# Performance work log

Measured on AMD Instinct MI355X. Metric: run time of the kernel, lower is better.

## Reference

```python
import jax, jax.numpy as jnp
import numpy as np

N_NODES = 50000
N_EDGES = 500000
IN_DIM = 128
H1, C1 = 4, 64   # layer1: heads=4, out=64, concat -> 256
H2, C2 = 1, 64   # layer2: heads=1, out=64


def setup_inputs() -> dict:
    key = jax.random.key(0)
    ks = jax.random.split(key, 16)
    p = lambda k, shp: (jax.random.normal(k, shp, dtype=jnp.float32) * 0.1)
    return {
        "x": jax.random.normal(ks[0], (N_NODES, IN_DIM), dtype=jnp.float32),
        "edge_index": jax.random.randint(ks[1], (2, N_EDGES), 0, N_NODES, dtype=jnp.int32),
        "edge_attr": jax.random.uniform(ks[2], (N_EDGES, 1), dtype=jnp.float32),
        # layer 1 params
        "W1": p(ks[3], (IN_DIM, H1 * C1)),
        "We1": p(ks[4], (1, H1 * C1)),
        "as1": p(ks[5], (H1, C1)),
        "ad1": p(ks[6], (H1, C1)),
        "ae1": p(ks[7], (H1, C1)),
        "b1": jnp.zeros((H1 * C1,), dtype=jnp.float32),
        # layer 2 params
        "W2": p(ks[8], (H1 * C1, H2 * C2)),
        "We2": p(ks[9], (1, H2 * C2)),
        "as2": p(ks[10], (H2, C2)),
        "ad2": p(ks[11], (H2, C2)),
        "ae2": p(ks[12], (H2, C2)),
        "b2": jnp.zeros((H2 * C2,), dtype=jnp.float32),
    }


def _add_self_loops(src, dst, edge_attr, n):
    # PyG fill_value='mean': loop edge_attr = mean of incoming edge attrs per node
    cnt = jax.ops.segment_sum(jnp.ones((src.shape[0],), edge_attr.dtype), dst, num_segments=n)
    loop_attr = jax.ops.segment_sum(edge_attr, dst, num_segments=n) / jnp.maximum(cnt, 1.0)[:, None]
    idx = jnp.arange(n, dtype=src.dtype)
    return (jnp.concatenate([src, idx]), jnp.concatenate([dst, idx]),
            jnp.concatenate([edge_attr, loop_attr], axis=0))


def _gat_conv(x, src, dst, edge_attr, W, We, a_src, a_dst, a_edge, bias, heads, out_ch):
    n = x.shape[0]
    h = (x @ W).reshape(n, heads, out_ch)                      # [N,H,C]
    e = (edge_attr @ We).reshape(-1, heads, out_ch)            # [E,H,C]
    alpha = ((h * a_src).sum(-1)[src]                          # gather src score
             + (h * a_dst).sum(-1)[dst]                        # gather dst score
             + (e * a_edge).sum(-1))                           # [E,H]
    alpha = jax.nn.leaky_relu(alpha, 0.2)
    m = jax.ops.segment_max(alpha, dst, num_segments=n)        # per-target max
    alpha = jnp.exp(alpha - m[dst])
    denom = jax.ops.segment_sum(alpha, dst, num_segments=n)
    alpha = alpha / (denom[dst] + 1e-16)
    out = jax.ops.segment_sum(h[src] * alpha[..., None], dst, num_segments=n)
    return out.reshape(n, heads * out_ch) + bias


def reference(x, edge_index, edge_attr, W1, We1, as1, ad1, ae1, b1,
              W2, We2, as2, ad2, ae2, b2):
    src, dst = edge_index[0], edge_index[1]
    src, dst, ea = _add_self_loops(src, dst, edge_attr, x.shape[0])
    h = jax.nn.elu(_gat_conv(x, src, dst, ea, W1, We1, as1, ad1, ae1, b1, H1, C1))
    return _gat_conv(h, src, dst, ea, W2, We2, as2, ad2, ae2, b2, H2, C2)
```

## Files before the change

kernel.cpp:

```cpp
#include <hip/hip_runtime.h>
#include <math.h>

#define NN 50000
#define NE 500000
#define DIM 128
#define HC1 256
#define HC2 64
#define BCAP 64
#define EPB 1024
#define NBUCKET ((NE + EPB - 1) / EPB)
#define GB ((NN + 63) / 64)
#define PSTRIDE 8

typedef __attribute__((ext_vector_type(8))) short short8;
typedef __attribute__((ext_vector_type(4))) float floatx4;


__device__ __forceinline__ unsigned short f2bf(float f) {
  unsigned int u = __float_as_uint(f);
  unsigned int r = (u + 0x7FFFu + ((u >> 16) & 1u)) >> 16;
  return (unsigned short)r;
}
__device__ __forceinline__ float bf2f(unsigned short s) {
  return __uint_as_float(((unsigned int)s) << 16);
}

__device__ __forceinline__ float waveReduce(float v) {
  v += __shfl_down(v, 32);
  v += __shfl_down(v, 16);
  v += __shfl_down(v, 8);
  v += __shfl_down(v, 4);
  v += __shfl_down(v, 2);
  v += __shfl_down(v, 1);
  return v;
}

__device__ __forceinline__ void decodeP(unsigned long long p, int& cn, float& lea) {
  int c = (int)(p >> 40);
  cn = (c < BCAP) ? c : BCAP;
  float asum = (float)(p & 0xFFFFFFFFFFULL) * (1.0f / 16777216.0f);
  lea = asum / fmaxf((float)c, 1.0f);
}


__global__ __launch_bounds__(256) void k_prep(const float* __restrict__ W1,
                                              const float* __restrict__ W2,
                                              const float* __restrict__ We1,
                                              const float* __restrict__ ae1,
                                              const float* __restrict__ We2,
                                              const float* __restrict__ ae2,
                                              unsigned short* __restrict__ W1T,
                                              unsigned short* __restrict__ W2T,
                                              float* __restrict__ ce) {
  int b = blockIdx.x, t = threadIdx.x;
  if (b < 128) {
    int idx = b * 256 + t;
    int n = idx >> 7, k = idx & 127;
    W1T[idx] = f2bf(W1[k * 256 + n]);
  } else if (b < 192) {
    int idx = (b - 128) * 256 + t;
    int n = idx >> 8, k = idx & 255;
    W2T[idx] = f2bf(W2[k * 64 + n]);
  } else {
    int h = t >> 6, lane = t & 63;
    float p = We1[h * 64 + lane] * ae1[h * 64 + lane];
    p = waveReduce(p);
    if (lane == 0) ce[h] = p;
    if (h == 0) {
      float q = We2[lane] * ae2[lane];
      q = waveReduce(q);
      if (lane == 0) ce[4] = q;
    }
  }
}


__global__ __launch_bounds__(256) void k_fused(const int* __restrict__ src,
                                               const int* __restrict__ dst,
                                               const float* __restrict__ ea,
                                               unsigned long long* __restrict__ P,
                                               unsigned int* __restrict__ ebuf,
                                               const float* __restrict__ x,
                                               const unsigned short* __restrict__ W1T,
                                               const float* __restrict__ as1,
                                               const float* __restrict__ ad1,
                                               unsigned short* __restrict__ h1b,
                                               float* __restrict__ ss1,
                                               float* __restrict__ sd1) {
  __shared__ unsigned short As[64 * 136];
  int t = threadIdx.x;

  if (blockIdx.x < NBUCKET) {
    int e0 = blockIdx.x * EPB + t;
    int dv[4]; float ev[4]; unsigned int sv[4]; bool ok[4];
#pragma unroll
    for (int k = 0; k < 4; k++) {
      int e = e0 + k * 256;
      ok[k] = (e < NE);
      int ee = ok[k] ? e : 0;
      dv[k] = dst[ee];
      ev[k] = ea[ee];
      sv[k] = (unsigned int)src[ee];
    }
    unsigned long long old[4];
#pragma unroll
    for (int k = 0; k < 4; k++) {
      if (ok[k]) {
        unsigned long long fx =
            (unsigned long long)(unsigned int)__float2uint_rn(ev[k] * 16777216.0f);
        old[k] = atomicAdd(&P[(unsigned long long)dv[k] * PSTRIDE], (1ULL << 40) | fx);
      }
    }
#pragma unroll
    for (int k = 0; k < 4; k++) {
      if (ok[k]) {
        int pos = (int)(old[k] >> 40);
        unsigned int ea16 = __float2uint_rn(ev[k] * 65536.0f);
        if (ea16 > 65535u) ea16 = 65535u;
        if (pos < BCAP)
          ebuf[dv[k] * BCAP + pos] = (ea16 << 16) | sv[k];
      }
    }
    return;
  }

  int wave = t >> 6, lane = t & 63;
  int q = lane >> 4, ln = lane & 15;
  int m0 = (blockIdx.x - NBUCKET) * 64;
  int n0 = wave * 64;

  short8 bfr[4][4];
#pragma unroll
  for (int c = 0; c < 4; c++)
#pragma unroll
    for (int ks = 0; ks < 4; ks++)
      bfr[c][ks] = *(const short8*)&W1T[(n0 + c * 16 + ln) * 128 + ks * 32 + q * 8];

#pragma unroll
  for (int rep = 0; rep < 8; rep++) {
    int chunk = t + 256 * rep;
    int m = chunk >> 5, kk = (chunk & 31) * 4;
    int gr = m0 + m;
    float4 v = (gr < NN) ? *(const float4*)&x[gr * DIM + kk]
                         : make_float4(0.f, 0.f, 0.f, 0.f);
    ushort4 o;
    o.x = f2bf(v.x); o.y = f2bf(v.y); o.z = f2bf(v.z); o.w = f2bf(v.w);
    *(ushort4*)&As[m * 136 + kk] = o;
  }
  __syncthreads();

  floatx4 acc[4][4];
#pragma unroll
  for (int r = 0; r < 4; r++)
#pragma unroll
    for (int c = 0; c < 4; c++) acc[r][c] = (floatx4){0.f, 0.f, 0.f, 0.f};

#pragma unroll
  for (int ks = 0; ks < 4; ks++) {
    short8 afr[4];
#pragma unroll
    for (int r = 0; r < 4; r++)
      afr[r] = *(const short8*)&As[(r * 16 + ln) * 136 + ks * 32 + q * 8];
#pragma unroll
    for (int r = 0; r < 4; r++)
#pragma unroll
      for (int c = 0; c < 4; c++)
        acc[r][c] = __builtin_amdgcn_mfma_f32_16x16x32_bf16(afr[r], bfr[c][ks], acc[r][c], 0, 0, 0);
  }

  float as1v[4], ad1v[4];
#pragma unroll
  for (int c = 0; c < 4; c++) {
    as1v[c] = as1[n0 + c * 16 + ln];
    ad1v[c] = ad1[n0 + c * 16 + ln];
  }

#pragma unroll
  for (int r = 0; r < 4; r++) {
#pragma unroll
    for (int i = 0; i < 4; i++) {
      int gm = m0 + r * 16 + q * 4 + i;
      if (gm < NN) {
#pragma unroll
        for (int c = 0; c < 4; c++)
          h1b[gm * HC1 + n0 + c * 16 + ln] = f2bf(acc[r][c][i]);
      }
      float ps = acc[r][0][i] * as1v[0];
      float pd = acc[r][0][i] * ad1v[0];
#pragma unroll
      for (int c = 1; c < 4; c++) {
        ps = fmaf(acc[r][c][i], as1v[c], ps);
        pd = fmaf(acc[r][c][i], ad1v[c], pd);
      }
#pragma unroll
      for (int m = 1; m < 16; m <<= 1) {
        ps += __shfl_xor(ps, m);
        pd += __shfl_xor(pd, m);
      }
      if (ln == 0 && gm < NN) {
        ss1[gm * 4 + wave] = ps;
        sd1[gm * 4 + wave] = pd;
      }
    }
  }
}

__global__ __launch_bounds__(256) void k_gemm2m(const unsigned short* __restrict__ out1b,
                                                const unsigned short* __restrict__ W2T,
                                                const float* __restrict__ as2,
                                                const float* __restrict__ ad2,
                                                unsigned short* __restrict__ h2b,
                                                float* __restrict__ ss2,
                                                float* __restrict__ sd2) {
  __shared__ unsigned short As[64 * 264];
  __shared__ float ssp[4][64], sdp[4][64];
  int t = threadIdx.x;
  int wave = t >> 6, lane = t & 63;
  int q = lane >> 4, ln = lane & 15;
  int m0 = blockIdx.x * 64;
  int n0 = wave * 16;

  short8 bfr[8];
#pragma unroll
  for (int ks = 0; ks < 8; ks++)
    bfr[ks] = *(const short8*)&W2T[(n0 + ln) * 256 + ks * 32 + q * 8];

  short8 zero8 = {0, 0, 0, 0, 0, 0, 0, 0};
#pragma unroll
  for (int rep = 0; rep < 8; rep++) {
    int chunk = t + 256 * rep;
    int m = chunk >> 5, kk = (chunk & 31) * 8;
    int gr = m0 + m;
    short8 vv = (gr < NN) ? *(const short8*)&out1b[gr * 256 + kk] : zero8;
    *(short8*)&As[m * 264 + kk] = vv;
  }
  __syncthreads();

  floatx4 acc[4];
#pragma unroll
  for (int r = 0; r < 4; r++) acc[r] = (floatx4){0.f, 0.f, 0.f, 0.f};

#pragma unroll
  for (int ks = 0; ks < 8; ks++) {
#pragma unroll
    for (int r = 0; r < 4; r++) {
      short8 afr = *(const short8*)&As[(r * 16 + ln) * 264 + ks * 32 + q * 8];
      acc[r] = __builtin_amdgcn_mfma_f32_16x16x32_bf16(afr, bfr[ks], acc[r], 0, 0, 0);
    }
  }

  float as2v = as2[n0 + ln], ad2v = ad2[n0 + ln];
#pragma unroll
  for (int r = 0; r < 4; r++) {
#pragma unroll
    for (int i = 0; i < 4; i++) {
      int gm = m0 + r * 16 + q * 4 + i;
      if (gm < NN) h2b[gm * HC2 + n0 + ln] = f2bf(acc[r][i]);
      float ps = acc[r][i] * as2v;
      float pd = acc[r][i] * ad2v;
#pragma unroll
      for (int m = 1; m < 16; m <<= 1) {
        ps += __shfl_xor(ps, m);
        pd += __shfl_xor(pd, m);
      }
      if (ln == 0) {
        ssp[wave][r * 16 + q * 4 + i] = ps;
        sdp[wave][r * 16 + q * 4 + i] = pd;
      }
    }
  }
  __syncthreads();
  if (t < 64) {
    int gm = m0 + t;
    if (gm < NN) {
      ss2[gm] = ssp[0][t] + ssp[1][t] + ssp[2][t] + ssp[3][t];
      sd2[gm] = sdp[0][t] + sdp[1][t] + sdp[2][t] + sdp[3][t];
    }
  }
}


__global__ __launch_bounds__(256) void k_agg1(const unsigned short* __restrict__ h1b,
                                              const unsigned long long* __restrict__ P,
                                              const unsigned int* __restrict__ ebuf,
                                              const float* __restrict__ ss1,
                                              const float* __restrict__ sd1,
                                              const float* __restrict__ ce,
                                              const float* __restrict__ b1,
                                              unsigned short* __restrict__ out1b) {
  int v = (blockIdx.x * blockDim.x + threadIdx.x) >> 6;
  int lane = threadIdx.x & 63;
  int h = lane >> 4;
  int c4 = lane * 4;
  int l16 = lane & 15;
  int vu = __builtin_amdgcn_readfirstlane(v);
  int cn; float lea;
  decodeP(P[(unsigned long long)vu * PSTRIDE], cn, lea);
  cn = __builtin_amdgcn_readfirstlane(cn);
  int beg = vu * BCAP;
  int end = beg + cn;
  float sdh = sd1[vu * 4 + h];
  float ceh = ce[h];
  float4 acc = make_float4(0.f, 0.f, 0.f, 0.f);
  float l = 0.f;

  for (int base = beg; base < end; base += 16) {
    unsigned int meta = ebuf[base + l16];
#pragma unroll
    for (int b4 = 0; b4 < 4; b4++) {
      if (base + b4 * 4 >= end) break;
      float ssv[4], ea4[4];
      ushort4 u[4];
      bool vld[4];
#pragma unroll
      for (int jj = 0; jj < 4; jj++) {
        int j = b4 * 4 + jj;
        bool val = (base + j < end);
        unsigned int m = __builtin_amdgcn_readlane(meta, j);
        int sj = val ? (int)(m & 0xFFFFu) : 0;
        ea4[jj] = (float)(m >> 16) * (1.0f / 65536.0f);
        vld[jj] = val;
        ssv[jj] = ss1[sj * 4 + h];
        u[jj] = *(const ushort4*)&h1b[sj * HC1 + c4];
      }
#pragma unroll
      for (int jj = 0; jj < 4; jj++) {
        float x = fmaf(ea4[jj], ceh, ssv[jj] + sdh);
        x = fmaxf(x, 0.2f * x);
        float a = vld[jj] ? __expf(x) : 0.f;
        l += a;
        acc.x = fmaf(a, bf2f(u[jj].x), acc.x);
        acc.y = fmaf(a, bf2f(u[jj].y), acc.y);
        acc.z = fmaf(a, bf2f(u[jj].z), acc.z);
        acc.w = fmaf(a, bf2f(u[jj].w), acc.w);
      }
    }
  }
  {
    float x = fmaf(lea, ceh, ss1[vu * 4 + h] + sdh);
    x = fmaxf(x, 0.2f * x);
    float a = __expf(x);
    ushort4 u = *(const ushort4*)&h1b[vu * HC1 + c4];
    l += a;
    acc.x = fmaf(a, bf2f(u.x), acc.x);
    acc.y = fmaf(a, bf2f(u.y), acc.y);
    acc.z = fmaf(a, bf2f(u.z), acc.z);
    acc.w = fmaf(a, bf2f(u.w), acc.w);
  }
  float inv = 1.f / (l + 1e-16f);
  float4 bv = *(const float4*)&b1[c4];
  float4 o;
  o.x = acc.x * inv + bv.x;
  o.y = acc.y * inv + bv.y;
  o.z = acc.z * inv + bv.z;
  o.w = acc.w * inv + bv.w;
  o.x = (o.x > 0.f) ? o.x : expm1f(o.x);
  o.y = (o.y > 0.f) ? o.y : expm1f(o.y);
  o.z = (o.z > 0.f) ? o.z : expm1f(o.z);
  o.w = (o.w > 0.f) ? o.w : expm1f(o.w);
  ushort4 ob;
  ob.x = f2bf(o.x); ob.y = f2bf(o.y); ob.z = f2bf(o.z); ob.w = f2bf(o.w);
  *(ushort4*)&out1b[vu * HC1 + c4] = ob;
}

__global__ __launch_bounds__(256) void k_agg2(const unsigned short* __restrict__ h2b,
                                              const unsigned long long* __restrict__ P,
                                              const unsigned int* __restrict__ ebuf,
                                              const float* __restrict__ ss2,
                                              const float* __restrict__ sd2,
                                              const float* __restrict__ ce,
                                              const float* __restrict__ b2,
                                              float* __restrict__ out) {
  int v = (blockIdx.x * blockDim.x + threadIdx.x) >> 6;
  int lane = threadIdx.x & 63;
  int g = lane >> 4;
  int c = lane & 15;
  int l16 = lane & 15;
  int vu = __builtin_amdgcn_readfirstlane(v);
  int cn; float lea;
  decodeP(P[(unsigned long long)vu * PSTRIDE], cn, lea);
  cn = __builtin_amdgcn_readfirstlane(cn);
  int beg = vu * BCAP;
  int end = beg + cn;
  float sdv = sd2[vu];
  float cev = ce[4];
  float4 acc = make_float4(0.f, 0.f, 0.f, 0.f);
  float l = 0.f;

  for (int base = beg; base < end; base += 16) {
    int nb = end - base;
    unsigned int meta = ebuf[base + l16];
    float ssv[4], eav[4];
    bool vld[4];
    ushort4 u[4];
#pragma unroll
    for (int sub = 0; sub < 4; sub++) {
      int j = sub * 4 + g;
      bool val = (j < nb);
      unsigned int m = (unsigned int)__shfl((int)meta, j);
      int sj = val ? (int)(m & 0xFFFFu) : 0;
      eav[sub] = (float)(m >> 16) * (1.0f / 65536.0f);
      vld[sub] = val;
      ssv[sub] = ss2[sj];
      u[sub] = *(const ushort4*)&h2b[sj * HC2 + c * 4];
    }
#pragma unroll
    for (int sub = 0; sub < 4; sub++) {
      float x = fmaf(eav[sub], cev, ssv[sub] + sdv);
      x = fmaxf(x, 0.2f * x);
      float a = vld[sub] ? __expf(x) : 0.f;
      l += a;
      acc.x = fmaf(a, bf2f(u[sub].x), acc.x);
      acc.y = fmaf(a, bf2f(u[sub].y), acc.y);
      acc.z = fmaf(a, bf2f(u[sub].z), acc.z);
      acc.w = fmaf(a, bf2f(u[sub].w), acc.w);
    }
  }
#pragma unroll
  for (int m = 16; m <= 32; m <<= 1) {
    acc.x += __shfl_xor(acc.x, m);
    acc.y += __shfl_xor(acc.y, m);
    acc.z += __shfl_xor(acc.z, m);
    acc.w += __shfl_xor(acc.w, m);
    l += __shfl_xor(l, m);
  }
  {
    float x = fmaf(lea, cev, ss2[vu] + sdv);
    x = fmaxf(x, 0.2f * x);
    float a = __expf(x);
    ushort4 us = *(const ushort4*)&h2b[vu * HC2 + c * 4];
    l += a;
    acc.x = fmaf(a, bf2f(us.x), acc.x);
    acc.y = fmaf(a, bf2f(us.y), acc.y);
    acc.z = fmaf(a, bf2f(us.z), acc.z);
    acc.w = fmaf(a, bf2f(us.w), acc.w);
  }
  if (g == 0) {
    float inv = 1.f / (l + 1e-16f);
    float4 bv = *(const float4*)&b2[c * 4];
    float4 o;
    o.x = acc.x * inv + bv.x;
    o.y = acc.y * inv + bv.y;
    o.z = acc.z * inv + bv.z;
    o.w = acc.w * inv + bv.w;
    *(float4*)&out[vu * HC2 + c * 4] = o;
  }
}


extern "C" void kernel_launch(void* const* d_in, const int* in_sizes, int n_in,
                              void* d_out, int out_size, void* d_ws, size_t ws_size,
                              hipStream_t stream) {
  const float* x   = (const float*)d_in[0];
  const int*   ei  = (const int*)d_in[1];
  const float* ea  = (const float*)d_in[2];
  const float* W1  = (const float*)d_in[3];
  const float* We1 = (const float*)d_in[4];
  const float* as1 = (const float*)d_in[5];
  const float* ad1 = (const float*)d_in[6];
  const float* ae1 = (const float*)d_in[7];
  const float* b1  = (const float*)d_in[8];
  const float* W2  = (const float*)d_in[9];
  const float* We2 = (const float*)d_in[10];
  const float* as2 = (const float*)d_in[11];
  const float* ad2 = (const float*)d_in[12];
  const float* ae2 = (const float*)d_in[13];
  const float* b2  = (const float*)d_in[14];
  const int* srcp = ei;
  const int* dstp = ei + NE;

  char* w = (char*)d_ws;
  unsigned long long* P = (unsigned long long*)(w + 0);
  float* ce      = (float*)(w + 3200064);
  float* ss1     = (float*)(w + 3200640);
  float* sd1     = (float*)(w + 4000640);
  float* ss2     = (float*)(w + 4800640);
  float* sd2     = (float*)(w + 5000640);
  unsigned int* ebuf = (unsigned int*)(w + 5200640);
  unsigned short* h1b   = (unsigned short*)(w + 18000640);
  unsigned short* out1b = (unsigned short*)(w + 43600640);
  unsigned short* h2b   = (unsigned short*)(w + 69200640);
  unsigned short* W1T   = (unsigned short*)(w + 75600640);
  unsigned short* W2T   = (unsigned short*)(w + 75666176);

  hipMemsetAsync(w, 0, 3200000, stream);

  k_prep<<<193, 256, 0, stream>>>(W1, W2, We1, ae1, We2, ae2, W1T, W2T, ce);
  k_fused<<<NBUCKET + GB, 256, 0, stream>>>(srcp, dstp, ea, P, ebuf,
                                            x, W1T, as1, ad1, h1b, ss1, sd1);

  k_agg1<<<(NN * 64 + 255) / 256, 256, 0, stream>>>(h1b, P, ebuf, ss1, sd1, ce, b1, out1b);

  k_gemm2m<<<(NN + 63) / 64, 256, 0, stream>>>(out1b, W2T, as2, ad2, h2b, ss2, sd2);
  k_agg2<<<(NN * 64 + 255) / 256, 256, 0, stream>>>(h2b, P, ebuf, ss2, sd2, ce, b2,
                                                    (float*)d_out);
}
```

Baseline: 226.9 us.

## Split bucket and GEMM kernels, use 32-bit counters, recompute self-loop mean in aggregation

Splits the fused bucketing/GEMM kernel into two separate launches. The 64-bit packed count+edge-attr atomic becomes a 32-bit count atomic, and the self-loop mean edge attribute is rebuilt in the aggregation kernels from the quantized bucket values. It also permutes the W1T column mapping so each lane stores four contiguous bf16 outputs with a single ushort4 write and loads its attention vectors as float4. The trade-offs are losing overlap between bucketing and GEMM, a slightly less precise self-loop attribute because it is averaged from 16-bit values, and extra reduction work in aggregation. Edges dropped beyond the bucket capacity no longer count toward the mean.

```diff
diff --git a/kernel.cpp b/kernel.cpp
--- a/kernel.cpp
+++ b/kernel.cpp
@@ -10,7 +10,7 @@
 #define EPB 1024
 #define NBUCKET ((NE + EPB - 1) / EPB)
 #define GB ((NN + 63) / 64)
-#define PSTRIDE 8
+#define CSTRIDE 16
 
 typedef __attribute__((ext_vector_type(8))) short short8;
 typedef __attribute__((ext_vector_type(4))) float floatx4;
@@ -33,13 +33,6 @@
   v += __shfl_down(v, 2);
   v += __shfl_down(v, 1);
   return v;
-}
-
-__device__ __forceinline__ void decodeP(unsigned long long p, int& cn, float& lea) {
-  int c = (int)(p >> 40);
-  cn = (c < BCAP) ? c : BCAP;
-  float asum = (float)(p & 0xFFFFFFFFFFULL) * (1.0f / 16777216.0f);
-  lea = asum / fmaxf((float)c, 1.0f);
 }
 
 
@@ -75,12 +68,41 @@
 }
 
 
-__global__ __launch_bounds__(256) void k_fused(const int* __restrict__ src,
-                                               const int* __restrict__ dst,
-                                               const float* __restrict__ ea,
-                                               unsigned long long* __restrict__ P,
-                                               unsigned int* __restrict__ ebuf,
-                                               const float* __restrict__ x,
+__global__ __launch_bounds__(256) void k_bucket(const int* __restrict__ src,
+                                                const int* __restrict__ dst,
+                                                const float* __restrict__ ea,
+                                                unsigned int* __restrict__ cnt,
+                                                unsigned int* __restrict__ ebuf) {
+  int t = threadIdx.x;
+  int e0 = blockIdx.x * EPB + t;
+  int dv[4]; float ev[4]; unsigned int sv[4]; bool ok[4];
+#pragma unroll
+  for (int k = 0; k < 4; k++) {
+    int e = e0 + k * 256;
+    ok[k] = (e < NE);
+    int ee = ok[k] ? e : 0;
+    dv[k] = dst[ee];
+    ev[k] = ea[ee];
+    sv[k] = (unsigned int)src[ee];
+  }
+  unsigned int old[4];
+#pragma unroll
+  for (int k = 0; k < 4; k++) {
+    if (ok[k]) old[k] = atomicAdd(&cnt[(unsigned long long)dv[k] * CSTRIDE], 1u);
+  }
+#pragma unroll
+  for (int k = 0; k < 4; k++) {
+    if (ok[k]) {
+      unsigned int ea16 = __float2uint_rn(ev[k] * 65536.0f);
+      if (ea16 > 65535u) ea16 = 65535u;
+      if (old[k] < BCAP)
+        ebuf[dv[k] * BCAP + old[k]] = (ea16 << 16) | sv[k];
+    }
+  }
+}
+
+
+__global__ __launch_bounds__(256) void k_gemm1(const float* __restrict__ x,
                                                const unsigned short* __restrict__ W1T,
                                                const float* __restrict__ as1,
                                                const float* __restrict__ ad1,
@@ -89,44 +111,9 @@
                                                float* __restrict__ sd1) {
   __shared__ unsigned short As[64 * 136];
   int t = threadIdx.x;
-
-  if (blockIdx.x < NBUCKET) {
-    int e0 = blockIdx.x * EPB + t;
-    int dv[4]; float ev[4]; unsigned int sv[4]; bool ok[4];
-#pragma unroll
-    for (int k = 0; k < 4; k++) {
-      int e = e0 + k * 256;
-      ok[k] = (e < NE);
-      int ee = ok[k] ? e : 0;
-      dv[k] = dst[ee];
-      ev[k] = ea[ee];
-      sv[k] = (unsigned int)src[ee];
-    }
-    unsigned long long old[4];
-#pragma unroll
-    for (int k = 0; k < 4; k++) {
-      if (ok[k]) {
-        unsigned long long fx =
-            (unsigned long long)(unsigned int)__float2uint_rn(ev[k] * 16777216.0f);
-        old[k] = atomicAdd(&P[(unsigned long long)dv[k] * PSTRIDE], (1ULL << 40) | fx);
-      }
-    }
-#pragma unroll
-    for (int k = 0; k < 4; k++) {
-      if (ok[k]) {
-        int pos = (int)(old[k] >> 40);
-        unsigned int ea16 = __float2uint_rn(ev[k] * 65536.0f);
-        if (ea16 > 65535u) ea16 = 65535u;
-        if (pos < BCAP)
-          ebuf[dv[k] * BCAP + pos] = (ea16 << 16) | sv[k];
-      }
-    }
-    return;
-  }
-
   int wave = t >> 6, lane = t & 63;
   int q = lane >> 4, ln = lane & 15;
-  int m0 = (blockIdx.x - NBUCKET) * 64;
+  int m0 = blockIdx.x * 64;
   int n0 = wave * 64;
 
   short8 bfr[4][4];
@@ -134,7 +121,7 @@
   for (int c = 0; c < 4; c++)
 #pragma unroll
     for (int ks = 0; ks < 4; ks++)
-      bfr[c][ks] = *(const short8*)&W1T[(n0 + c * 16 + ln) * 128 + ks * 32 + q * 8];
+      bfr[c][ks] = *(const short8*)&W1T[(n0 + ln * 4 + c) * 128 + ks * 32 + q * 8];
 
 #pragma unroll
   for (int rep = 0; rep < 8; rep++) {
@@ -168,12 +155,8 @@
         acc[r][c] = __builtin_amdgcn_mfma_f32_16x16x32_bf16(afr[r], bfr[c][ks], acc[r][c], 0, 0, 0);
   }
 
-  float as1v[4], ad1v[4];
-#pragma unroll
-  for (int c = 0; c < 4; c++) {
-    as1v[c] = as1[n0 + c * 16 + ln];
-    ad1v[c] = ad1[n0 + c * 16 + ln];
-  }
+  float4 a4 = *(const float4*)&as1[n0 + ln * 4];
+  float4 d4 = *(const float4*)&ad1[n0 + ln * 4];
 
 #pragma unroll
   for (int r = 0; r < 4; r++) {
@@ -181,17 +164,21 @@
     for (int i = 0; i < 4; i++) {
       int gm = m0 + r * 16 + q * 4 + i;
       if (gm < NN) {
-#pragma unroll
-        for (int c = 0; c < 4; c++)
-          h1b[gm * HC1 + n0 + c * 16 + ln] = f2bf(acc[r][c][i]);
-      }
-      float ps = acc[r][0][i] * as1v[0];
-      float pd = acc[r][0][i] * ad1v[0];
-#pragma unroll
-      for (int c = 1; c < 4; c++) {
-        ps = fmaf(acc[r][c][i], as1v[c], ps);
-        pd = fmaf(acc[r][c][i], ad1v[c], pd);
-      }
+        ushort4 o;
+        o.x = f2bf(acc[r][0][i]);
+        o.y = f2bf(acc[r][1][i]);
+        o.z = f2bf(acc[r][2][i]);
+        o.w = f2bf(acc[r][3][i]);
+        *(ushort4*)&h1b[gm * HC1 + n0 + ln * 4] = o;
+      }
+      float ps = acc[r][0][i] * a4.x;
+      float pd = acc[r][0][i] * d4.x;
+      ps = fmaf(acc[r][1][i], a4.y, ps);
+      pd = fmaf(acc[r][1][i], d4.y, pd);
+      ps = fmaf(acc[r][2][i], a4.z, ps);
+      pd = fmaf(acc[r][2][i], d4.z, pd);
+      ps = fmaf(acc[r][3][i], a4.w, ps);
+      pd = fmaf(acc[r][3][i], d4.w, pd);
 #pragma unroll
       for (int m = 1; m < 16; m <<= 1) {
         ps += __shfl_xor(ps, m);
@@ -281,7 +268,7 @@
 
 
 __global__ __launch_bounds__(256) void k_agg1(const unsigned short* __restrict__ h1b,
-                                              const unsigned long long* __restrict__ P,
+                                              const unsigned int* __restrict__ cnt,
                                               const unsigned int* __restrict__ ebuf,
                                               const float* __restrict__ ss1,
                                               const float* __restrict__ sd1,
@@ -294,8 +281,8 @@
   int c4 = lane * 4;
   int l16 = lane & 15;
   int vu = __builtin_amdgcn_readfirstlane(v);
-  int cn; float lea;
-  decodeP(P[(unsigned long long)vu * PSTRIDE], cn, lea);
+  unsigned int craw = cnt[(unsigned long long)vu * CSTRIDE];
+  int cn = (craw < BCAP) ? (int)craw : BCAP;
   cn = __builtin_amdgcn_readfirstlane(cn);
   int beg = vu * BCAP;
   int end = beg + cn;
@@ -303,6 +290,7 @@
   float ceh = ce[h];
   float4 acc = make_float4(0.f, 0.f, 0.f, 0.f);
   float l = 0.f;
+  float easum = 0.f;
 
   for (int base = beg; base < end; base += 16) {
     unsigned int meta = ebuf[base + l16];
@@ -325,6 +313,7 @@
       }
 #pragma unroll
       for (int jj = 0; jj < 4; jj++) {
+        easum += vld[jj] ? ea4[jj] : 0.f;
         float x = fmaf(ea4[jj], ceh, ssv[jj] + sdh);
         x = fmaxf(x, 0.2f * x);
         float a = vld[jj] ? __expf(x) : 0.f;
@@ -337,6 +326,7 @@
     }
   }
   {
+    float lea = easum / fmaxf((float)cn, 1.0f);
     float x = fmaf(lea, ceh, ss1[vu * 4 + h] + sdh);
     x = fmaxf(x, 0.2f * x);
     float a = __expf(x);
@@ -364,7 +354,7 @@
 }
 
 __global__ __launch_bounds__(256) void k_agg2(const unsigned short* __restrict__ h2b,
-                                              const unsigned long long* __restrict__ P,
+                                              const unsigned int* __restrict__ cnt,
                                               const unsigned int* __restrict__ ebuf,
                                               const float* __restrict__ ss2,
                                               const float* __restrict__ sd2,
@@ -377,8 +367,8 @@
   int c = lane & 15;
   int l16 = lane & 15;
   int vu = __builtin_amdgcn_readfirstlane(v);
-  int cn; float lea;
-  decodeP(P[(unsigned long long)vu * PSTRIDE], cn, lea);
+  unsigned int craw = cnt[(unsigned long long)vu * CSTRIDE];
+  int cn = (craw < BCAP) ? (int)craw : BCAP;
   cn = __builtin_amdgcn_readfirstlane(cn);
   int beg = vu * BCAP;
   int end = beg + cn;
@@ -386,6 +376,7 @@
   float cev = ce[4];
   float4 acc = make_float4(0.f, 0.f, 0.f, 0.f);
   float l = 0.f;
+  float easum = 0.f;
 
   for (int base = beg; base < end; base += 16) {
     int nb = end - base;
@@ -406,6 +397,7 @@
     }
 #pragma unroll
     for (int sub = 0; sub < 4; sub++) {
+      easum += vld[sub] ? eav[sub] : 0.f;
       float x = fmaf(eav[sub], cev, ssv[sub] + sdv);
       x = fmaxf(x, 0.2f * x);
       float a = vld[sub] ? __expf(x) : 0.f;
@@ -423,8 +415,10 @@
     acc.z += __shfl_xor(acc.z, m);
     acc.w += __shfl_xor(acc.w, m);
     l += __shfl_xor(l, m);
+    easum += __shfl_xor(easum, m);
   }
   {
+    float lea = easum / fmaxf((float)cn, 1.0f);
     float x = fmaf(lea, cev, ss2[vu] + sdv);
     x = fmaxf(x, 0.2f * x);
     float a = __expf(x);
@@ -470,7 +464,7 @@
   const int* dstp = ei + NE;
 
   char* w = (char*)d_ws;
-  unsigned long long* P = (unsigned long long*)(w + 0);
+  unsigned int* cnt = (unsigned int*)(w + 0);
   float* ce      = (float*)(w + 3200064);
   float* ss1     = (float*)(w + 3200640);
   float* sd1     = (float*)(w + 4000640);
@@ -486,12 +480,12 @@
   hipMemsetAsync(w, 0, 3200000, stream);
 
   k_prep<<<193, 256, 0, stream>>>(W1, W2, We1, ae1, We2, ae2, W1T, W2T, ce);
-  k_fused<<<NBUCKET + GB, 256, 0, stream>>>(srcp, dstp, ea, P, ebuf,
-                                            x, W1T, as1, ad1, h1b, ss1, sd1);
-
-  k_agg1<<<(NN * 64 + 255) / 256, 256, 0, stream>>>(h1b, P, ebuf, ss1, sd1, ce, b1, out1b);
+  k_bucket<<<NBUCKET, 256, 0, stream>>>(srcp, dstp, ea, cnt, ebuf);
+  k_gemm1<<<GB, 256, 0, stream>>>(x, W1T, as1, ad1, h1b, ss1, sd1);
+
+  k_agg1<<<(NN * 64 + 255) / 256, 256, 0, stream>>>(h1b, cnt, ebuf, ss1, sd1, ce, b1, out1b);
 
   k_gemm2m<<<(NN + 63) / 64, 256, 0, stream>>>(out1b, W2T, as2, ad2, h2b, ss2, sd2);
-  k_agg2<<<(NN * 64 + 255) / 256, 256, 0, stream>>>(h2b, P, ebuf, ss2, sd2, ce, b2,
+  k_agg2<<<(NN * 64 + 255) / 256, 256, 0, stream>>>(h2b, cnt, ebuf, ss2, sd2, ce, b2,
                                                     (float*)d_out);
 }
```

Result: no change. 227.3 us (+0.2%).
